# Kernel tuning notes

Hardware: AMD Instinct MI355X
Metric: run time of the kernel (lower is better)

The kernel has to match this reference:

```python
import jax, jax.numpy as jnp
import numpy as np

N_NODES = 100000
N_EDGES = 1250000
IN_DIM = 12
HID = 64
N_LAYERS = 3
LN_EPS = 1e-5
LEAKY_SLOPE = 0.01


def _layer_norm(x, g, b):
    mu = jnp.mean(x, axis=-1, keepdims=True)
    var = jnp.var(x, axis=-1, keepdims=True)
    return (x - mu) * jax.lax.rsqrt(var + LN_EPS) * g + b


def setup_inputs() -> dict:
    key = jax.random.key(0)
    ks = jax.random.split(key, 16)
    s = 0.1  # param init scale
    return {
        "x": jax.random.normal(ks[0], (N_NODES, IN_DIM), jnp.float32),
        "edge_index": jax.random.randint(ks[1], (2, N_EDGES), 0, N_NODES, jnp.int64),
        "edge_weight": jax.random.uniform(ks[2], (N_EDGES,), jnp.float32),
        "in_W": s * jax.random.normal(ks[3], (IN_DIM, HID), jnp.float32),
        "in_b": jnp.zeros((HID,), jnp.float32),
        "lin_W": s * jax.random.normal(ks[4], (N_LAYERS, HID, HID), jnp.float32),
        "lin_b": jnp.zeros((N_LAYERS, HID), jnp.float32),
        "att_W": s * jax.random.normal(ks[5], (N_LAYERS, 2 * HID, 1), jnp.float32),
        "att_b": jnp.zeros((N_LAYERS, 1), jnp.float32),
        "ln_g": jnp.ones((N_LAYERS, HID), jnp.float32),
        "ln_b": jnp.zeros((N_LAYERS, HID), jnp.float32),
        "out1_W": s * jax.random.normal(ks[6], (HID, HID // 2), jnp.float32),
        "out1_b": jnp.zeros((HID // 2,), jnp.float32),
        "out2_W": s * jax.random.normal(ks[7], (HID // 2, 1), jnp.float32),
        "out2_b": jnp.zeros((1,), jnp.float32),
    }


def reference(x, edge_index, edge_weight, in_W, in_b, lin_W, lin_b,
              att_W, att_b, ln_g, ln_b, out1_W, out1_b, out2_W, out2_b):
    row, col = edge_index[0], edge_index[1]
    h = x @ in_W + in_b  # [N, HID]
    for i in range(N_LAYERS):
        hl = h @ lin_W[i] + lin_b[i]  # [N, HID]
        h_i = hl[row]  # [E, HID]
        h_j = hl[col]  # [E, HID]
        att_in = jnp.concatenate([h_i, h_j], axis=-1)  # [E, 2*HID]
        scores = jax.nn.leaky_relu(att_in @ att_W[i] + att_b[i], LEAKY_SLOPE)  # [E, 1]
        scores = jax.nn.softmax(scores, axis=0)  # global softmax over edges (as in source)
        scores = scores * edge_weight[:, None]
        messages = scores * h_j  # [E, HID]
        agg = jax.ops.segment_sum(messages, row, num_segments=N_NODES)
        h_new = jax.nn.relu(hl + agg)
        h_new = _layer_norm(h_new, ln_g[i], ln_b[i])
        # dropout is identity in eval mode
        h = h + h_new
    z = jax.nn.relu(h @ out1_W + out1_b)
    return jax.nn.sigmoid(z @ out2_W + out2_b)  # [N, 1]
```

## Files before the change

### kernel.cpp

```cpp
#include <hip/hip_runtime.h>
#include <hip/hip_fp8.h>
#include <math.h>

#define N_NODES 100000
#define N_EDGES 1250000
#define IN_DIM 12
#define HID 64
#define N_LAYERS 3
#define LN_EPS 1e-5f
#define SLOPE 0.01f

#define NODE_BLOCKS ((N_NODES + 3) / 4)
#define EDGE_TBLOCKS ((N_EDGES + 255) / 256)
#define SCAN_BLOCKS ((N_NODES + 1023) / 1024)
#define MFMA_BLOCKS ((N_NODES + 63) / 64)
#define NEDGE_BLOCKS ((N_NODES + 255) / 256)

#define BUCKETS 256
#define BUCKET_NODES 391
#define P1_EDGES 4096
#define P1_BLOCKS ((N_EDGES + P1_EDGES - 1) / P1_EDGES)

#define LEW_SCALE 2048.0f
#define LEW_INV (1.0f / 2048.0f)

typedef short bf16x8 __attribute__((ext_vector_type(8)));
typedef float f32x4 __attribute__((ext_vector_type(4)));

static __device__ __forceinline__ unsigned short f2bf(float f) {
  union { float f; unsigned int u; } v; v.f = f;
  unsigned int r = v.u + 0x7FFFu + ((v.u >> 16) & 1u);
  return (unsigned short)(r >> 16);
}
static __device__ __forceinline__ unsigned char f2e4(float f) {
  return __hip_fp8_e4m3(f).__x;
}
static __device__ __forceinline__ float e42f(unsigned char b) {
  __hip_fp8_e4m3 d; d.__x = b;
  return (float)d;
}

__global__ void k_in_proj(const float* __restrict__ x,
                          const float* __restrict__ W,
                          const float* __restrict__ b,
                          float* __restrict__ h) {
  __shared__ float sW[IN_DIM * HID];
  for (int i = threadIdx.x; i < IN_DIM * HID; i += blockDim.x) sW[i] = W[i];
  __syncthreads();
  int wave = threadIdx.x >> 6, lane = threadIdx.x & 63;
  int n = blockIdx.x * 4 + wave;
  if (n >= N_NODES) return;
  float acc = b[lane];
#pragma unroll
  for (int k = 0; k < IN_DIM; ++k)
    acc += x[n * IN_DIM + k] * sW[k * HID + lane];
  h[n * HID + lane] = acc;
}

__global__ void k_hist(const int* __restrict__ ei, int* __restrict__ deg) {
  int e = blockIdx.x * 256 + threadIdx.x;
  if (e >= N_EDGES) return;
  atomicAdd(&deg[ei[e]], 1);
}

__global__ void k_blocksums(const int* __restrict__ deg, int* __restrict__ bsum) {
  __shared__ int sm[1024];
  int i = blockIdx.x * 1024 + threadIdx.x;
  sm[threadIdx.x] = (i < N_NODES) ? deg[i] : 0;
  __syncthreads();
  for (int st = 512; st > 0; st >>= 1) {
    if (threadIdx.x < st) sm[threadIdx.x] += sm[threadIdx.x + st];
    __syncthreads();
  }
  if (threadIdx.x == 0) bsum[blockIdx.x] = sm[0];
}

__global__ void k_scan_bsums(int* __restrict__ bsum, int nb) {
  __shared__ int sm[128];
  int v = (threadIdx.x < nb) ? bsum[threadIdx.x] : 0;
  sm[threadIdx.x] = v;
  __syncthreads();
  for (int st = 1; st < 128; st <<= 1) {
    int t = (threadIdx.x >= st) ? sm[threadIdx.x - st] : 0;
    __syncthreads();
    sm[threadIdx.x] += t;
    __syncthreads();
  }
  if (threadIdx.x < nb) bsum[threadIdx.x] = sm[threadIdx.x] - v;
}

__global__ void k_scan_final(const int* __restrict__ deg, const int* __restrict__ bsum,
                             int* __restrict__ rowptr) {
  __shared__ int sm[1024];
  int i = blockIdx.x * 1024 + threadIdx.x;
  int v = (i < N_NODES) ? deg[i] : 0;
  sm[threadIdx.x] = v;
  __syncthreads();
  for (int st = 1; st < 1024; st <<= 1) {
    int t = (threadIdx.x >= st) ? sm[threadIdx.x - st] : 0;
    __syncthreads();
    sm[threadIdx.x] += t;
    __syncthreads();
  }
  int excl = sm[threadIdx.x] - v + bsum[blockIdx.x];
  if (i < N_NODES) rowptr[i] = excl;
}

__global__ void k_bcur(const int* __restrict__ rowptr, unsigned* __restrict__ gbcur) {
  int b = threadIdx.x;
  if (b < BUCKETS) gbcur[b] = (unsigned)rowptr[b * BUCKET_NODES];
}

__global__ void k_fill_p1(const int* __restrict__ ei, const float* __restrict__ ew,
                          unsigned* __restrict__ gbcur,
                          unsigned long long* __restrict__ tmp) {
  __shared__ unsigned cnt[BUCKETS], gbase[BUCKETS], lofs[BUCKETS];
  int t = threadIdx.x;
  cnt[t] = 0;
  __syncthreads();
  int base = blockIdx.x * P1_EDGES;
#pragma unroll
  for (int i = 0; i < 16; ++i) {
    int e = base + i * 256 + t;
    if (e < N_EDGES) atomicAdd(&cnt[(unsigned)ei[e] / BUCKET_NODES], 1u);
  }
  __syncthreads();
  {
    unsigned c = cnt[t];
    gbase[t] = c ? atomicAdd(&gbcur[t], c) : 0u;
    lofs[t] = 0;
  }
  __syncthreads();
#pragma unroll
  for (int i = 0; i < 16; ++i) {
    int e = base + i * 256 + t;
    if (e < N_EDGES) {
      unsigned r = (unsigned)ei[e], c = (unsigned)ei[N_EDGES + e];
      float lew = __logf(ew[e]);
      lew = fmaxf(lew, -15.9995f);
      unsigned q = (unsigned)(-lew * LEW_SCALE + 0.5f);
      if (q > 32767u) q = 32767u;
      unsigned b = r / BUCKET_NODES;
      unsigned idx = atomicAdd(&lofs[b], 1u);
      tmp[gbase[b] + idx] = ((unsigned long long)r << 32)
                          | ((unsigned long long)c << 15) | q;
    }
  }
}

__global__ void k_fill_p2(const int* __restrict__ rowptr,
                          const unsigned long long* __restrict__ tmp,
                          unsigned* __restrict__ packed) {
  __shared__ int lcur[BUCKET_NODES];
  int b = blockIdx.x, t = threadIdx.x;
  int nb0 = b * BUCKET_NODES;
  int nb1 = min(nb0 + BUCKET_NODES, N_NODES);
  int nn = nb1 - nb0;
  for (int j = t; j < nn; j += 256) lcur[j] = rowptr[nb0 + j];
  __syncthreads();
  int beg = rowptr[nb0];
  int end = (nb1 < N_NODES) ? rowptr[nb1] : N_EDGES;
  for (int i = beg + t; i < end; i += 256) {
    unsigned long long rec = tmp[i];
    int r = (int)(rec >> 32);
    int pos = atomicAdd(&lcur[r - nb0], 1);
    packed[pos] = (unsigned)(rec & 0xFFFFFFFFu);
  }
}

__global__ void k_prep(const float* __restrict__ lin_W,
                       const float* __restrict__ lin_b,
                       const float* __restrict__ att_W,
                       float* __restrict__ uvec,
                       float* __restrict__ ucst) {
  int l = blockIdx.x, j = threadIdx.x;
  const float* Wl = lin_W + l * HID * HID;
  const float* a1 = att_W + l * 2 * HID;
  const float* a2 = a1 + HID;
  float s1 = 0.f, s2 = 0.f;
  for (int c = 0; c < HID; ++c) {
    float w = Wl[j * HID + c];
    s1 += w * a1[c];
    s2 += w * a2[c];
  }
  uvec[l * 128 + j] = s1;
  uvec[l * 128 + 64 + j] = s2;
  float t1 = lin_b[l * HID + j] * a1[j];
  float t2 = lin_b[l * HID + j] * a2[j];
#pragma unroll
  for (int off = 32; off > 0; off >>= 1) {
    t1 += __shfl_xor(t1, off, 64);
    t2 += __shfl_xor(t2, off, 64);
  }
  if (j == 0) { ucst[l * 2] = t1; ucst[l * 2 + 1] = t2; }
}

__global__ void k_lin_mfma(const float* __restrict__ h,
                           const float* __restrict__ W,
                           const float* __restrict__ bias,
                           const float* __restrict__ uvec,
                           const float* __restrict__ ucst,
                           float* __restrict__ hl,
                           unsigned char* __restrict__ hl8,
                           float* __restrict__ alpha1,
                           float* __restrict__ alpha2) {
  __shared__ unsigned short Wt[HID * 72];
  for (int idx = threadIdx.x; idx < HID * HID; idx += 256) {
    int k = idx >> 6, n = idx & 63;
    Wt[n * 72 + k] = f2bf(W[idx]);
  }
  __syncthreads();

  int wave = threadIdx.x >> 6, lane = threadIdx.x & 63;
  int g = lane >> 4, r = lane & 15;
  int nb = blockIdx.x * 64 + wave * 16;
  int row = nb + r;
  bool rowok = row < N_NODES;

  f32x4 f0 = {0,0,0,0}, f1 = {0,0,0,0}, f2v = {0,0,0,0}, f3 = {0,0,0,0};
  if (rowok) {
    const float* hrow = h + (size_t)row * HID;
    f0  = *(const f32x4*)(hrow + g * 8);
    f1  = *(const f32x4*)(hrow + g * 8 + 4);
    f2v = *(const f32x4*)(hrow + 32 + g * 8);
    f3  = *(const f32x4*)(hrow + 32 + g * 8 + 4);
  }
  bf16x8 a0, a1f;
#pragma unroll
  for (int i = 0; i < 4; ++i) {
    a0[i]      = (short)f2bf(f0[i]);
    a0[i + 4]  = (short)f2bf(f1[i]);
    a1f[i]     = (short)f2bf(f2v[i]);
    a1f[i + 4] = (short)f2bf(f3[i]);
  }

  f32x4 acc[4] = {{0,0,0,0},{0,0,0,0},{0,0,0,0},{0,0,0,0}};
#pragma unroll
  for (int nt = 0; nt < 4; ++nt) {
    bf16x8 b0 = *(const bf16x8*)&Wt[(nt * 16 + r) * 72 + g * 8];
    bf16x8 b1 = *(const bf16x8*)&Wt[(nt * 16 + r) * 72 + 32 + g * 8];
    acc[nt] = __builtin_amdgcn_mfma_f32_16x16x32_bf16(a0, b0, acc[nt], 0, 0, 0);
    acc[nt] = __builtin_amdgcn_mfma_f32_16x16x32_bf16(a1f, b1, acc[nt], 0, 0, 0);
  }

  {
    const float* u1 = uvec;
    const float* u2 = uvec + HID;
    f32x4 ua = *(const f32x4*)(u1 + g * 8),      ub = *(const f32x4*)(u1 + g * 8 + 4);
    f32x4 uc = *(const f32x4*)(u1 + 32 + g * 8), ud = *(const f32x4*)(u1 + 32 + g * 8 + 4);
    float p1 = f0[0]*ua[0]+f0[1]*ua[1]+f0[2]*ua[2]+f0[3]*ua[3]
             + f1[0]*ub[0]+f1[1]*ub[1]+f1[2]*ub[2]+f1[3]*ub[3]
             + f2v[0]*uc[0]+f2v[1]*uc[1]+f2v[2]*uc[2]+f2v[3]*uc[3]
             + f3[0]*ud[0]+f3[1]*ud[1]+f3[2]*ud[2]+f3[3]*ud[3];
    ua = *(const f32x4*)(u2 + g * 8);      ub = *(const f32x4*)(u2 + g * 8 + 4);
    uc = *(const f32x4*)(u2 + 32 + g * 8); ud = *(const f32x4*)(u2 + 32 + g * 8 + 4);
    float p2 = f0[0]*ua[0]+f0[1]*ua[1]+f0[2]*ua[2]+f0[3]*ua[3]
             + f1[0]*ub[0]+f1[1]*ub[1]+f1[2]*ub[2]+f1[3]*ub[3]
             + f2v[0]*uc[0]+f2v[1]*uc[1]+f2v[2]*uc[2]+f2v[3]*uc[3]
             + f3[0]*ud[0]+f3[1]*ud[1]+f3[2]*ud[2]+f3[3]*ud[3];
    p1 += __shfl_xor(p1, 16, 64); p1 += __shfl_xor(p1, 32, 64);
    p2 += __shfl_xor(p2, 16, 64); p2 += __shfl_xor(p2, 32, 64);
    if (g == 0 && rowok) {
      alpha1[row] = p1 + ucst[0];
      alpha2[row] = p2 + ucst[1];
    }
  }

#pragma unroll
  for (int nt = 0; nt < 4; ++nt) {
    float bv = bias[nt * 16 + r];
#pragma unroll
    for (int reg = 0; reg < 4; ++reg) {
      int n2 = nb + g * 4 + reg;
      if (n2 < N_NODES) {
        float v = acc[nt][reg] + bv;
        hl[(size_t)n2 * HID + nt * 16 + r] = v;
        hl8[(size_t)n2 * HID + nt * 16 + r] = f2e4(v);
      }
    }
  }
}

__global__ void k_edge(const int* __restrict__ rowptr,
                       const int* __restrict__ deg,
                       const unsigned* __restrict__ packed,
                       const float* __restrict__ alpha1,
                       const float* __restrict__ alpha2,
                       const float* __restrict__ attB,
                       float* __restrict__ slw,
                       float* __restrict__ pmax,
                       float* __restrict__ psum,
                       int* __restrict__ counter,
                       float* __restrict__ red) {
  int t = threadIdx.x;
  int n = blockIdx.x * 256 + t;
  float m = -INFINITY, sum = 0.f;
  if (n < N_NODES) {
    float a1 = alpha1[n] + attB[0];
    int beg = rowptr[n];
    int end = beg + deg[n];
    for (int p = beg; p < end; ++p) {
      unsigned u = packed[p];
      float sc = a1 + alpha2[u >> 15];
      sc = sc > 0.f ? sc : SLOPE * sc;
      slw[p] = sc - (float)(u & 0x7FFFu) * LEW_INV;
      if (sc > m) { sum *= __expf(m - sc); m = sc; }
      sum += __expf(sc - m);
    }
  }
  __shared__ float smax[256], ssum[256];
  __shared__ bool last;
  smax[t] = m; ssum[t] = sum;
  __syncthreads();
  for (int st = 128; st > 0; st >>= 1) {
    if (t < st) {
      float ma = smax[t], mb = smax[t + st];
      float sa = ssum[t], sb = ssum[t + st];
      float mm = fmaxf(ma, mb);
      float ss = 0.f;
      if (mm != -INFINITY)
        ss = (ma == -INFINITY ? 0.f : sa * __expf(ma - mm))
           + (mb == -INFINITY ? 0.f : sb * __expf(mb - mm));
      smax[t] = mm; ssum[t] = ss;
    }
    __syncthreads();
  }
  if (t == 0) {
    pmax[blockIdx.x] = smax[0];
    psum[blockIdx.x] = ssum[0];
    __threadfence();
    int old = atomicAdd(counter, 1);
    last = (old == (int)gridDim.x - 1);
  }
  __syncthreads();
  if (!last) return;
  __threadfence();
  volatile const float* vpm = pmax;
  volatile const float* vps = psum;
  float m2 = -INFINITY, s2 = 0.f;
  for (int i = t; i < (int)gridDim.x; i += 256) {
    float mb = vpm[i], sb = vps[i];
    if (mb != -INFINITY) {
      if (mb > m2) { s2 *= __expf(m2 - mb); m2 = mb; }
      s2 += sb * __expf(mb - m2);
    }
  }
  __syncthreads();
  smax[t] = m2; ssum[t] = s2;
  __syncthreads();
  for (int st = 128; st > 0; st >>= 1) {
    if (t < st) {
      float ma = smax[t], mb = smax[t + st];
      float sa = ssum[t], sb = ssum[t + st];
      float mm = fmaxf(ma, mb);
      float ss = 0.f;
      if (mm != -INFINITY)
        ss = (ma == -INFINITY ? 0.f : sa * __expf(ma - mm))
           + (mb == -INFINITY ? 0.f : sb * __expf(mb - mm));
      smax[t] = mm; ssum[t] = ss;
    }
    __syncthreads();
  }
  if (t == 0) {
    red[0] = smax[0];
    red[1] = ssum[0];
    *counter = 0;
  }
}

__global__ void k_exp2(float* __restrict__ slw, const float* __restrict__ red) {
  int e = blockIdx.x * 256 + threadIdx.x;
  if (e < N_EDGES) slw[e] = __expf(slw[e] - red[0]);
}

__global__ void k_agg_update(const int* __restrict__ rowptr,
                             const int* __restrict__ deg,
                             const unsigned* __restrict__ packed,
                             const float* __restrict__ w,
                             const float* __restrict__ red,
                             const float* __restrict__ hl,
                             const unsigned char* __restrict__ hl8,
                             const float* __restrict__ gam,
                             const float* __restrict__ bet,
                             float* __restrict__ h) {
  int wave = threadIdx.x >> 6, lane = threadIdx.x & 63;
  int n = blockIdx.x * 4 + wave;
  if (n >= N_NODES) return;
  int g = lane >> 4, q = lane & 15;
  int beg = rowptr[n];
  int end = beg + deg[n];

  float a0 = 0.f, a1 = 0.f, a2 = 0.f, a3 = 0.f;
  for (int k = beg; k < end; k += 8) {
    int ke0 = k + g, ke1 = k + 4 + g;
    bool v0 = ke0 < end, v1 = ke1 < end;
    unsigned u0 = packed[v0 ? ke0 : beg];
    unsigned u1 = packed[v1 ? ke1 : beg];
    float w0 = v0 ? w[ke0] : 0.f;
    float w1 = v1 ? w[ke1] : 0.f;
    unsigned d0 = *(const unsigned*)(hl8 + (size_t)(u0 >> 15) * HID + q * 4);
    unsigned d1 = *(const unsigned*)(hl8 + (size_t)(u1 >> 15) * HID + q * 4);
    a0 += w0 * e42f(d0 & 0xffu)         + w1 * e42f(d1 & 0xffu);
    a1 += w0 * e42f((d0 >> 8) & 0xffu)  + w1 * e42f((d1 >> 8) & 0xffu);
    a2 += w0 * e42f((d0 >> 16) & 0xffu) + w1 * e42f((d1 >> 16) & 0xffu);
    a3 += w0 * e42f(d0 >> 24)           + w1 * e42f(d1 >> 24);
  }
  a0 += __shfl_xor(a0, 16, 64); a0 += __shfl_xor(a0, 32, 64);
  a1 += __shfl_xor(a1, 16, 64); a1 += __shfl_xor(a1, 32, 64);
  a2 += __shfl_xor(a2, 16, 64); a2 += __shfl_xor(a2, 32, 64);
  a3 += __shfl_xor(a3, 16, 64); a3 += __shfl_xor(a3, 32, 64);

  float inv = 1.0f / red[1];
  const float* hlrow = hl + (size_t)n * HID + q * 4;
  float v0 = fmaxf(hlrow[0] + a0 * inv, 0.f);
  float v1 = fmaxf(hlrow[1] + a1 * inv, 0.f);
  float v2 = fmaxf(hlrow[2] + a2 * inv, 0.f);
  float v3 = fmaxf(hlrow[3] + a3 * inv, 0.f);

  float ms = v0 + v1 + v2 + v3;
  ms += __shfl_xor(ms, 1, 64); ms += __shfl_xor(ms, 2, 64);
  ms += __shfl_xor(ms, 4, 64); ms += __shfl_xor(ms, 8, 64);
  float m = ms * (1.0f / HID);
  float d0 = v0 - m, d1 = v1 - m, d2 = v2 - m, d3 = v3 - m;
  float vs = d0 * d0 + d1 * d1 + d2 * d2 + d3 * d3;
  vs += __shfl_xor(vs, 1, 64); vs += __shfl_xor(vs, 2, 64);
  vs += __shfl_xor(vs, 4, 64); vs += __shfl_xor(vs, 8, 64);
  float rs = rsqrtf(vs * (1.0f / HID) + LN_EPS);

  if (g == 0) {
    float* hrow = h + (size_t)n * HID + q * 4;
    f32x4 hv = *(const f32x4*)hrow;
    f32x4 gv = *(const f32x4*)(gam + q * 4);
    f32x4 bv = *(const f32x4*)(bet + q * 4);
    f32x4 o;
    o[0] = hv[0] + d0 * rs * gv[0] + bv[0];
    o[1] = hv[1] + d1 * rs * gv[1] + bv[1];
    o[2] = hv[2] + d2 * rs * gv[2] + bv[2];
    o[3] = hv[3] + d3 * rs * gv[3] + bv[3];
    *(f32x4*)hrow = o;
  }
}

__global__ void k_out_mfma(const float* __restrict__ h,
                           const float* __restrict__ W1,
                           const float* __restrict__ b1,
                           const float* __restrict__ W2,
                           const float* __restrict__ b2,
                           float* __restrict__ out) {
  __shared__ unsigned short W1t[32 * 72];
  __shared__ float sW2[32];
  for (int idx = threadIdx.x; idx < HID * 32; idx += 256) {
    int k = idx >> 5, m = idx & 31;
    W1t[m * 72 + k] = f2bf(W1[idx]);
  }
  if (threadIdx.x < 32) sW2[threadIdx.x] = W2[threadIdx.x];
  __syncthreads();

  int wave = threadIdx.x >> 6, lane = threadIdx.x & 63;
  int g = lane >> 4, r = lane & 15;
  int nb = blockIdx.x * 64 + wave * 16;
  int row = nb + r;
  bool rowok = row < N_NODES;

  f32x4 f0 = {0,0,0,0}, f1 = {0,0,0,0}, f2v = {0,0,0,0}, f3 = {0,0,0,0};
  if (rowok) {
    const float* hrow = h + (size_t)row * HID;
    f0  = *(const f32x4*)(hrow + g * 8);
    f1  = *(const f32x4*)(hrow + g * 8 + 4);
    f2v = *(const f32x4*)(hrow + 32 + g * 8);
    f3  = *(const f32x4*)(hrow + 32 + g * 8 + 4);
  }
  bf16x8 a0, a1f;
#pragma unroll
  for (int i = 0; i < 4; ++i) {
    a0[i]      = (short)f2bf(f0[i]);
    a0[i + 4]  = (short)f2bf(f1[i]);
    a1f[i]     = (short)f2bf(f2v[i]);
    a1f[i + 4] = (short)f2bf(f3[i]);
  }

  f32x4 acc[2] = {{0,0,0,0},{0,0,0,0}};
#pragma unroll
  for (int mt = 0; mt < 2; ++mt) {
    bf16x8 b0 = *(const bf16x8*)&W1t[(mt * 16 + r) * 72 + g * 8];
    bf16x8 b1v = *(const bf16x8*)&W1t[(mt * 16 + r) * 72 + 32 + g * 8];
    acc[mt] = __builtin_amdgcn_mfma_f32_16x16x32_bf16(a0, b0, acc[mt], 0, 0, 0);
    acc[mt] = __builtin_amdgcn_mfma_f32_16x16x32_bf16(a1f, b1v, acc[mt], 0, 0, 0);
  }

  float part[4];
#pragma unroll
  for (int reg = 0; reg < 4; ++reg) {
    float p = 0.f;
#pragma unroll
    for (int mt = 0; mt < 2; ++mt) {
      float z = acc[mt][reg] + b1[mt * 16 + r];
      p += fmaxf(z, 0.f) * sW2[mt * 16 + r];
    }
    p += __shfl_xor(p, 1, 64);
    p += __shfl_xor(p, 2, 64);
    p += __shfl_xor(p, 4, 64);
    p += __shfl_xor(p, 8, 64);
    part[reg] = p;
  }
  if (r == 0) {
    float bb = b2[0];
#pragma unroll
    for (int reg = 0; reg < 4; ++reg) {
      int n2 = nb + g * 4 + reg;
      if (n2 < N_NODES)
        out[n2] = 1.0f / (1.0f + expf(-(part[reg] + bb)));
    }
  }
}

extern "C" void kernel_launch(void* const* d_in, const int* in_sizes, int n_in,
                              void* d_out, int out_size, void* d_ws, size_t ws_size,
                              hipStream_t stream) {
  const float* x      = (const float*)d_in[0];
  const int*   ei     = (const int*)d_in[1];
  const float* ew     = (const float*)d_in[2];
  const float* in_W   = (const float*)d_in[3];
  const float* in_b   = (const float*)d_in[4];
  const float* lin_W  = (const float*)d_in[5];
  const float* lin_b  = (const float*)d_in[6];
  const float* att_W  = (const float*)d_in[7];
  const float* att_b  = (const float*)d_in[8];
  const float* ln_g   = (const float*)d_in[9];
  const float* ln_b   = (const float*)d_in[10];
  const float* out1_W = (const float*)d_in[11];
  const float* out1_b = (const float*)d_in[12];
  const float* out2_W = (const float*)d_in[13];
  const float* out2_b = (const float*)d_in[14];
  float* out = (float*)d_out;

  float* ws = (float*)d_ws;
  float* h            = ws;
  float* hl           = ws + 6400000;
  unsigned char* hl8  = (unsigned char*)(ws + 12800000);
  unsigned long long* tmp = (unsigned long long*)(ws + 14500000);
  unsigned* packed    = (unsigned*)(ws + 17000000);
  float* slw          = ws + 18250000;
  int* deg            = (int*)(ws + 19500000);
  int* counter        = deg + N_NODES;
  int* rowptr         = (int*)(ws + 19601000);
  float* alpha1       = ws + 19702000;
  float* alpha2       = ws + 19803000;
  float* pmax         = ws + 19904000;
  float* psum         = ws + 19906000;
  float* red          = ws + 19908000;
  float* uvec         = ws + 19909000;
  float* ucst         = ws + 19910000;
  int* bsum           = (int*)(ws + 19911000);
  unsigned* gbcur     = (unsigned*)(ws + 19912000);

  hipMemsetAsync(deg, 0, (N_NODES + 1) * sizeof(int), stream);
  k_hist<<<EDGE_TBLOCKS, 256, 0, stream>>>(ei, deg);
  k_blocksums<<<SCAN_BLOCKS, 1024, 0, stream>>>(deg, bsum);
  k_scan_bsums<<<1, 128, 0, stream>>>(bsum, SCAN_BLOCKS);
  k_scan_final<<<SCAN_BLOCKS, 1024, 0, stream>>>(deg, bsum, rowptr);
  k_bcur<<<1, 256, 0, stream>>>(rowptr, gbcur);
  k_fill_p1<<<P1_BLOCKS, 256, 0, stream>>>(ei, ew, gbcur, tmp);
  k_fill_p2<<<BUCKETS, 256, 0, stream>>>(rowptr, tmp, packed);

  k_prep<<<N_LAYERS, 64, 0, stream>>>(lin_W, lin_b, att_W, uvec, ucst);
  k_in_proj<<<NODE_BLOCKS, 256, 0, stream>>>(x, in_W, in_b, h);

  for (int i = 0; i < N_LAYERS; ++i) {
    k_lin_mfma<<<MFMA_BLOCKS, 256, 0, stream>>>(h, lin_W + i * HID * HID, lin_b + i * HID,
                                                uvec + i * 128, ucst + i * 2,
                                                hl, hl8, alpha1, alpha2);
    k_edge<<<NEDGE_BLOCKS, 256, 0, stream>>>(rowptr, deg, packed, alpha1, alpha2,
                                             att_b + i, slw, pmax, psum, counter, red);
    k_exp2<<<EDGE_TBLOCKS, 256, 0, stream>>>(slw, red);
    k_agg_update<<<NODE_BLOCKS, 256, 0, stream>>>(rowptr, deg, packed, slw, red,
                                                  hl, hl8, ln_g + i * HID, ln_b + i * HID, h);
  }

  k_out_mfma<<<MFMA_BLOCKS, 256, 0, stream>>>(h, out1_W, out1_b, out2_W, out2_b, out);
}
```

Measured before the change: 444.0 us.

## Fuse bucket-cursor init into scan, vectorize exp, unroll aggregation, double MFMA tiles

Drops the separate k_bcur kernel by writing bucket cursors from the final scan kernel. k_exp2 now handles four floats per thread. The aggregation gather loop is unrolled to four edges per group and uses packed fp8-to-f32 conversion when the builtin is available. The linear MFMA kernel processes two 64-row tiles per block, so the shared-memory weight staging is paid once per 128 rows. Together these aim to cut launch overhead, per-edge instruction count and redundant weight conversion, at the cost of more register pressure and fewer blocks.

```diff
diff --git a/kernel.cpp b/kernel.cpp
--- a/kernel.cpp
+++ b/kernel.cpp
@@ -13,7 +13,8 @@
 #define NODE_BLOCKS ((N_NODES + 3) / 4)
 #define EDGE_TBLOCKS ((N_EDGES + 255) / 256)
 #define SCAN_BLOCKS ((N_NODES + 1023) / 1024)
-#define MFMA_BLOCKS ((N_NODES + 63) / 64)
+#define MFMA_BLOCKS2 ((N_NODES + 127) / 128)
+#define OUT_BLOCKS ((N_NODES + 63) / 64)
 #define NEDGE_BLOCKS ((N_NODES + 255) / 256)
 
 #define BUCKETS 256
@@ -26,6 +27,13 @@
 
 typedef short bf16x8 __attribute__((ext_vector_type(8)));
 typedef float f32x4 __attribute__((ext_vector_type(4)));
+typedef float f32x2 __attribute__((ext_vector_type(2)));
+
+#if defined(__has_builtin)
+#if __has_builtin(__builtin_amdgcn_cvt_pk_f32_fp8)
+#define HAVE_PK_FP8 1
+#endif
+#endif
 
 static __device__ __forceinline__ unsigned short f2bf(float f) {
   union { float f; unsigned int u; } v; v.f = f;
@@ -90,7 +98,7 @@
 }
 
 __global__ void k_scan_final(const int* __restrict__ deg, const int* __restrict__ bsum,
-                             int* __restrict__ rowptr) {
+                             int* __restrict__ rowptr, unsigned* __restrict__ gbcur) {
   __shared__ int sm[1024];
   int i = blockIdx.x * 1024 + threadIdx.x;
   int v = (i < N_NODES) ? deg[i] : 0;
@@ -103,12 +111,11 @@
     __syncthreads();
   }
   int excl = sm[threadIdx.x] - v + bsum[blockIdx.x];
-  if (i < N_NODES) rowptr[i] = excl;
-}
-
-__global__ void k_bcur(const int* __restrict__ rowptr, unsigned* __restrict__ gbcur) {
-  int b = threadIdx.x;
-  if (b < BUCKETS) gbcur[b] = (unsigned)rowptr[b * BUCKET_NODES];
+  if (i < N_NODES) {
+    rowptr[i] = excl;
+    int bb = i / BUCKET_NODES;
+    if (i - bb * BUCKET_NODES == 0) gbcur[bb] = (unsigned)excl;
+  }
 }
 
 __global__ void k_fill_p1(const int* __restrict__ ei, const float* __restrict__ ew,
@@ -213,69 +220,74 @@
 
   int wave = threadIdx.x >> 6, lane = threadIdx.x & 63;
   int g = lane >> 4, r = lane & 15;
-  int nb = blockIdx.x * 64 + wave * 16;
-  int row = nb + r;
-  bool rowok = row < N_NODES;
-
-  f32x4 f0 = {0,0,0,0}, f1 = {0,0,0,0}, f2v = {0,0,0,0}, f3 = {0,0,0,0};
-  if (rowok) {
-    const float* hrow = h + (size_t)row * HID;
-    f0  = *(const f32x4*)(hrow + g * 8);
-    f1  = *(const f32x4*)(hrow + g * 8 + 4);
-    f2v = *(const f32x4*)(hrow + 32 + g * 8);
-    f3  = *(const f32x4*)(hrow + 32 + g * 8 + 4);
-  }
-  bf16x8 a0, a1f;
-#pragma unroll
-  for (int i = 0; i < 4; ++i) {
-    a0[i]      = (short)f2bf(f0[i]);
-    a0[i + 4]  = (short)f2bf(f1[i]);
-    a1f[i]     = (short)f2bf(f2v[i]);
-    a1f[i + 4] = (short)f2bf(f3[i]);
-  }
-
-  f32x4 acc[4] = {{0,0,0,0},{0,0,0,0},{0,0,0,0},{0,0,0,0}};
-#pragma unroll
-  for (int nt = 0; nt < 4; ++nt) {
-    bf16x8 b0 = *(const bf16x8*)&Wt[(nt * 16 + r) * 72 + g * 8];
-    bf16x8 b1 = *(const bf16x8*)&Wt[(nt * 16 + r) * 72 + 32 + g * 8];
-    acc[nt] = __builtin_amdgcn_mfma_f32_16x16x32_bf16(a0, b0, acc[nt], 0, 0, 0);
-    acc[nt] = __builtin_amdgcn_mfma_f32_16x16x32_bf16(a1f, b1, acc[nt], 0, 0, 0);
-  }
-
-  {
-    const float* u1 = uvec;
-    const float* u2 = uvec + HID;
-    f32x4 ua = *(const f32x4*)(u1 + g * 8),      ub = *(const f32x4*)(u1 + g * 8 + 4);
-    f32x4 uc = *(const f32x4*)(u1 + 32 + g * 8), ud = *(const f32x4*)(u1 + 32 + g * 8 + 4);
-    float p1 = f0[0]*ua[0]+f0[1]*ua[1]+f0[2]*ua[2]+f0[3]*ua[3]
-             + f1[0]*ub[0]+f1[1]*ub[1]+f1[2]*ub[2]+f1[3]*ub[3]
-             + f2v[0]*uc[0]+f2v[1]*uc[1]+f2v[2]*uc[2]+f2v[3]*uc[3]
-             + f3[0]*ud[0]+f3[1]*ud[1]+f3[2]*ud[2]+f3[3]*ud[3];
-    ua = *(const f32x4*)(u2 + g * 8);      ub = *(const f32x4*)(u2 + g * 8 + 4);
-    uc = *(const f32x4*)(u2 + 32 + g * 8); ud = *(const f32x4*)(u2 + 32 + g * 8 + 4);
-    float p2 = f0[0]*ua[0]+f0[1]*ua[1]+f0[2]*ua[2]+f0[3]*ua[3]
-             + f1[0]*ub[0]+f1[1]*ub[1]+f1[2]*ub[2]+f1[3]*ub[3]
-             + f2v[0]*uc[0]+f2v[1]*uc[1]+f2v[2]*uc[2]+f2v[3]*uc[3]
-             + f3[0]*ud[0]+f3[1]*ud[1]+f3[2]*ud[2]+f3[3]*ud[3];
-    p1 += __shfl_xor(p1, 16, 64); p1 += __shfl_xor(p1, 32, 64);
-    p2 += __shfl_xor(p2, 16, 64); p2 += __shfl_xor(p2, 32, 64);
-    if (g == 0 && rowok) {
-      alpha1[row] = p1 + ucst[0];
-      alpha2[row] = p2 + ucst[1];
-    }
-  }
-
-#pragma unroll
-  for (int nt = 0; nt < 4; ++nt) {
-    float bv = bias[nt * 16 + r];
-#pragma unroll
-    for (int reg = 0; reg < 4; ++reg) {
-      int n2 = nb + g * 4 + reg;
-      if (n2 < N_NODES) {
-        float v = acc[nt][reg] + bv;
-        hl[(size_t)n2 * HID + nt * 16 + r] = v;
-        hl8[(size_t)n2 * HID + nt * 16 + r] = f2e4(v);
+
+#pragma unroll
+  for (int tile = 0; tile < 2; ++tile) {
+    int nb = blockIdx.x * 128 + tile * 64 + wave * 16;
+    int row = nb + r;
+    bool rowok = row < N_NODES;
+    if (nb >= N_NODES) break;
+
+    f32x4 f0 = {0,0,0,0}, f1 = {0,0,0,0}, f2v = {0,0,0,0}, f3 = {0,0,0,0};
+    if (rowok) {
+      const float* hrow = h + (size_t)row * HID;
+      f0  = *(const f32x4*)(hrow + g * 8);
+      f1  = *(const f32x4*)(hrow + g * 8 + 4);
+      f2v = *(const f32x4*)(hrow + 32 + g * 8);
+      f3  = *(const f32x4*)(hrow + 32 + g * 8 + 4);
+    }
+    bf16x8 a0, a1f;
+#pragma unroll
+    for (int i = 0; i < 4; ++i) {
+      a0[i]      = (short)f2bf(f0[i]);
+      a0[i + 4]  = (short)f2bf(f1[i]);
+      a1f[i]     = (short)f2bf(f2v[i]);
+      a1f[i + 4] = (short)f2bf(f3[i]);
+    }
+
+    f32x4 acc[4] = {{0,0,0,0},{0,0,0,0},{0,0,0,0},{0,0,0,0}};
+#pragma unroll
+    for (int nt = 0; nt < 4; ++nt) {
+      bf16x8 b0 = *(const bf16x8*)&Wt[(nt * 16 + r) * 72 + g * 8];
+      bf16x8 b1 = *(const bf16x8*)&Wt[(nt * 16 + r) * 72 + 32 + g * 8];
+      acc[nt] = __builtin_amdgcn_mfma_f32_16x16x32_bf16(a0, b0, acc[nt], 0, 0, 0);
+      acc[nt] = __builtin_amdgcn_mfma_f32_16x16x32_bf16(a1f, b1, acc[nt], 0, 0, 0);
+    }
+
+    {
+      const float* u1 = uvec;
+      const float* u2 = uvec + HID;
+      f32x4 ua = *(const f32x4*)(u1 + g * 8),      ub = *(const f32x4*)(u1 + g * 8 + 4);
+      f32x4 uc = *(const f32x4*)(u1 + 32 + g * 8), ud = *(const f32x4*)(u1 + 32 + g * 8 + 4);
+      float p1 = f0[0]*ua[0]+f0[1]*ua[1]+f0[2]*ua[2]+f0[3]*ua[3]
+               + f1[0]*ub[0]+f1[1]*ub[1]+f1[2]*ub[2]+f1[3]*ub[3]
+               + f2v[0]*uc[0]+f2v[1]*uc[1]+f2v[2]*uc[2]+f2v[3]*uc[3]
+               + f3[0]*ud[0]+f3[1]*ud[1]+f3[2]*ud[2]+f3[3]*ud[3];
+      ua = *(const f32x4*)(u2 + g * 8);      ub = *(const f32x4*)(u2 + g * 8 + 4);
+      uc = *(const f32x4*)(u2 + 32 + g * 8); ud = *(const f32x4*)(u2 + 32 + g * 8 + 4);
+      float p2 = f0[0]*ua[0]+f0[1]*ua[1]+f0[2]*ua[2]+f0[3]*ua[3]
+               + f1[0]*ub[0]+f1[1]*ub[1]+f1[2]*ub[2]+f1[3]*ub[3]
+               + f2v[0]*uc[0]+f2v[1]*uc[1]+f2v[2]*uc[2]+f2v[3]*uc[3]
+               + f3[0]*ud[0]+f3[1]*ud[1]+f3[2]*ud[2]+f3[3]*ud[3];
+      p1 += __shfl_xor(p1, 16, 64); p1 += __shfl_xor(p1, 32, 64);
+      p2 += __shfl_xor(p2, 16, 64); p2 += __shfl_xor(p2, 32, 64);
+      if (g == 0 && rowok) {
+        alpha1[row] = p1 + ucst[0];
+        alpha2[row] = p2 + ucst[1];
+      }
+    }
+
+#pragma unroll
+    for (int nt = 0; nt < 4; ++nt) {
+      float bv = bias[nt * 16 + r];
+#pragma unroll
+      for (int reg = 0; reg < 4; ++reg) {
+        int n2 = nb + g * 4 + reg;
+        if (n2 < N_NODES) {
+          float v = acc[nt][reg] + bv;
+          hl[(size_t)n2 * HID + nt * 16 + r] = v;
+          hl8[(size_t)n2 * HID + nt * 16 + r] = f2e4(v);
+        }
       }
     }
   }
@@ -368,9 +380,17 @@
   }
 }
 
-__global__ void k_exp2(float* __restrict__ slw, const float* __restrict__ red) {
-  int e = blockIdx.x * 256 + threadIdx.x;
-  if (e < N_EDGES) slw[e] = __expf(slw[e] - red[0]);
+__global__ void k_exp2(f32x4* __restrict__ slw, const float* __restrict__ red) {
+  int i = blockIdx.x * 256 + threadIdx.x;
+  int nvec = (N_EDGES + 3) / 4;
+  if (i >= nvec) return;
+  float M = red[0];
+  f32x4 v = slw[i];
+  v[0] = __expf(v[0] - M);
+  v[1] = __expf(v[1] - M);
+  v[2] = __expf(v[2] - M);
+  v[3] = __expf(v[3] - M);
+  slw[i] = v;
 }
 
 __global__ void k_agg_update(const int* __restrict__ rowptr,
@@ -391,19 +411,44 @@
   int end = beg + deg[n];
 
   float a0 = 0.f, a1 = 0.f, a2 = 0.f, a3 = 0.f;
-  for (int k = beg; k < end; k += 8) {
-    int ke0 = k + g, ke1 = k + 4 + g;
-    bool v0 = ke0 < end, v1 = ke1 < end;
+  for (int k = beg; k < end; k += 16) {
+    int ke0 = k + g, ke1 = k + 4 + g, ke2 = k + 8 + g, ke3 = k + 12 + g;
+    bool v0 = ke0 < end, v1 = ke1 < end, v2 = ke2 < end, v3 = ke3 < end;
     unsigned u0 = packed[v0 ? ke0 : beg];
     unsigned u1 = packed[v1 ? ke1 : beg];
+    unsigned u2 = packed[v2 ? ke2 : beg];
+    unsigned u3 = packed[v3 ? ke3 : beg];
     float w0 = v0 ? w[ke0] : 0.f;
     float w1 = v1 ? w[ke1] : 0.f;
+    float w2 = v2 ? w[ke2] : 0.f;
+    float w3 = v3 ? w[ke3] : 0.f;
     unsigned d0 = *(const unsigned*)(hl8 + (size_t)(u0 >> 15) * HID + q * 4);
     unsigned d1 = *(const unsigned*)(hl8 + (size_t)(u1 >> 15) * HID + q * 4);
-    a0 += w0 * e42f(d0 & 0xffu)         + w1 * e42f(d1 & 0xffu);
-    a1 += w0 * e42f((d0 >> 8) & 0xffu)  + w1 * e42f((d1 >> 8) & 0xffu);
-    a2 += w0 * e42f((d0 >> 16) & 0xffu) + w1 * e42f((d1 >> 16) & 0xffu);
-    a3 += w0 * e42f(d0 >> 24)           + w1 * e42f(d1 >> 24);
+    unsigned d2 = *(const unsigned*)(hl8 + (size_t)(u2 >> 15) * HID + q * 4);
+    unsigned d3 = *(const unsigned*)(hl8 + (size_t)(u3 >> 15) * HID + q * 4);
+#ifdef HAVE_PK_FP8
+    f32x2 l0 = __builtin_amdgcn_cvt_pk_f32_fp8((int)d0, 0);
+    f32x2 h0 = __builtin_amdgcn_cvt_pk_f32_fp8((int)d0, 1);
+    f32x2 l1 = __builtin_amdgcn_cvt_pk_f32_fp8((int)d1, 0);
+    f32x2 h1 = __builtin_amdgcn_cvt_pk_f32_fp8((int)d1, 1);
+    f32x2 l2 = __builtin_amdgcn_cvt_pk_f32_fp8((int)d2, 0);
+    f32x2 h2 = __builtin_amdgcn_cvt_pk_f32_fp8((int)d2, 1);
+    f32x2 l3 = __builtin_amdgcn_cvt_pk_f32_fp8((int)d3, 0);
+    f32x2 h3 = __builtin_amdgcn_cvt_pk_f32_fp8((int)d3, 1);
+    a0 += w0 * l0[0] + w1 * l1[0] + w2 * l2[0] + w3 * l3[0];
+    a1 += w0 * l0[1] + w1 * l1[1] + w2 * l2[1] + w3 * l3[1];
+    a2 += w0 * h0[0] + w1 * h1[0] + w2 * h2[0] + w3 * h3[0];
+    a3 += w0 * h0[1] + w1 * h1[1] + w2 * h2[1] + w3 * h3[1];
+#else
+    a0 += w0 * e42f(d0 & 0xffu) + w1 * e42f(d1 & 0xffu)
+        + w2 * e42f(d2 & 0xffu) + w3 * e42f(d3 & 0xffu);
+    a1 += w0 * e42f((d0 >> 8) & 0xffu) + w1 * e42f((d1 >> 8) & 0xffu)
+        + w2 * e42f((d2 >> 8) & 0xffu) + w3 * e42f((d3 >> 8) & 0xffu);
+    a2 += w0 * e42f((d0 >> 16) & 0xffu) + w1 * e42f((d1 >> 16) & 0xffu)
+        + w2 * e42f((d2 >> 16) & 0xffu) + w3 * e42f((d3 >> 16) & 0xffu);
+    a3 += w0 * e42f(d0 >> 24) + w1 * e42f(d1 >> 24)
+        + w2 * e42f(d2 >> 24) + w3 * e42f(d3 >> 24);
+#endif
   }
   a0 += __shfl_xor(a0, 16, 64); a0 += __shfl_xor(a0, 32, 64);
   a1 += __shfl_xor(a1, 16, 64); a1 += __shfl_xor(a1, 32, 64);
@@ -558,8 +603,7 @@
   k_hist<<<EDGE_TBLOCKS, 256, 0, stream>>>(ei, deg);
   k_blocksums<<<SCAN_BLOCKS, 1024, 0, stream>>>(deg, bsum);
   k_scan_bsums<<<1, 128, 0, stream>>>(bsum, SCAN_BLOCKS);
-  k_scan_final<<<SCAN_BLOCKS, 1024, 0, stream>>>(deg, bsum, rowptr);
-  k_bcur<<<1, 256, 0, stream>>>(rowptr, gbcur);
+  k_scan_final<<<SCAN_BLOCKS, 1024, 0, stream>>>(deg, bsum, rowptr, gbcur);
   k_fill_p1<<<P1_BLOCKS, 256, 0, stream>>>(ei, ew, gbcur, tmp);
   k_fill_p2<<<BUCKETS, 256, 0, stream>>>(rowptr, tmp, packed);
 
@@ -567,15 +611,15 @@
   k_in_proj<<<NODE_BLOCKS, 256, 0, stream>>>(x, in_W, in_b, h);
 
   for (int i = 0; i < N_LAYERS; ++i) {
-    k_lin_mfma<<<MFMA_BLOCKS, 256, 0, stream>>>(h, lin_W + i * HID * HID, lin_b + i * HID,
-                                                uvec + i * 128, ucst + i * 2,
-                                                hl, hl8, alpha1, alpha2);
+    k_lin_mfma<<<MFMA_BLOCKS2, 256, 0, stream>>>(h, lin_W + i * HID * HID, lin_b + i * HID,
+                                                 uvec + i * 128, ucst + i * 2,
+                                                 hl, hl8, alpha1, alpha2);
     k_edge<<<NEDGE_BLOCKS, 256, 0, stream>>>(rowptr, deg, packed, alpha1, alpha2,
                                              att_b + i, slw, pmax, psum, counter, red);
-    k_exp2<<<EDGE_TBLOCKS, 256, 0, stream>>>(slw, red);
+    k_exp2<<<(((N_EDGES + 3) / 4) + 255) / 256, 256, 0, stream>>>((f32x4*)slw, red);
     k_agg_update<<<NODE_BLOCKS, 256, 0, stream>>>(rowptr, deg, packed, slw, red,
                                                   hl, hl8, ln_g + i * HID, ln_b + i * HID, h);
   }
 
-  k_out_mfma<<<MFMA_BLOCKS, 256, 0, stream>>>(h, out1_W, out1_b, out2_W, out2_b, out);
-}
+  k_out_mfma<<<OUT_BLOCKS, 256, 0, stream>>>(h, out1_W, out1_b, out2_W, out2_b, out);
+}
```

Result: faster. 430.9 us (-3.0%).
